# Performance work log

Measured on AMD Instinct MI355X. Metric: run time of the kernel, lower is better.

Reference implementation:

```python
import jax, jax.numpy as jnp
import numpy as np

B = 512          # number of drug-combination graphs (batch)
MAX_LEN = 128    # static padding for to_dense_batch
D_DRUG = 256     # drug_in_features (kdim = vdim)
D_CELL = 1024    # cell_in_features
H = 16           # nheads
HD = 64          # h (per-head dim)
E = H * HD       # embed_dim = 1024


def setup_inputs() -> dict:
    key = jax.random.key(0)
    ks = jax.random.split(key, 12)
    N = 32768
    x_nodes = jax.random.normal(ks[0], (N, D_DRUG), dtype=jnp.float32)
    guide = jnp.sort(jax.random.randint(ks[1], (N,), 0, B)).astype(jnp.int64)
    cell = jax.random.normal(ks[2], (B, D_CELL), dtype=jnp.float32)
    s = 0.02
    return {
        "x_nodes": x_nodes,
        "cell": cell,
        "Wq": jax.random.normal(ks[3], (E, E), dtype=jnp.float32) * s,
        "bq": jnp.zeros((E,), dtype=jnp.float32),
        "Wk": jax.random.normal(ks[4], (E, D_DRUG), dtype=jnp.float32) * s,
        "bk": jnp.zeros((E,), dtype=jnp.float32),
        "Wv": jax.random.normal(ks[5], (E, D_DRUG), dtype=jnp.float32) * s,
        "bv": jnp.zeros((E,), dtype=jnp.float32),
        "Wo": jax.random.normal(ks[6], (E, E), dtype=jnp.float32) * s,
        "bo": jnp.zeros((E,), dtype=jnp.float32),
        "Wc": jax.random.normal(ks[7], (E, D_CELL), dtype=jnp.float32) * s,
        "bc": jnp.zeros((E,), dtype=jnp.float32),
        "guide": guide,
    }


def _to_dense_batch(x_nodes, guide):
    # Faithful torch_geometric.to_dense_batch with static MAX_LEN padding.
    N = x_nodes.shape[0]
    ones = jnp.ones((N,), dtype=jnp.int32)
    counts = jax.ops.segment_sum(ones, guide, num_segments=B)      # [B]
    starts = jnp.cumsum(counts) - counts                            # [B]
    pos = jnp.arange(N, dtype=jnp.int32) - starts[guide]            # rank within segment
    dense = jnp.zeros((B, MAX_LEN, x_nodes.shape[1]), x_nodes.dtype).at[guide, pos].set(x_nodes)
    mask = jnp.zeros((B, MAX_LEN), dtype=bool).at[guide, pos].set(True)
    return dense, mask


def reference(x_nodes, cell, Wq, bq, Wk, bk, Wv, bv, Wo, bo, Wc, bc, guide):
    drug_key, mask = _to_dense_batch(x_nodes, guide)                # [B,M,D_DRUG], [B,M]
    # cell_query_fc then MHA q-projection (single query per graph)
    cq = cell @ Wc.T + bc                                           # [B,E]
    q = (cq @ Wq.T + bq).reshape(B, H, HD) * (HD ** -0.5)           # [B,H,hd]
    k = (drug_key @ Wk.T + bk).reshape(B, MAX_LEN, H, HD)           # [B,M,H,hd]
    v = (drug_key @ Wv.T + bv).reshape(B, MAX_LEN, H, HD)
    scores = jnp.einsum('bhd,bmhd->bhm', q, k)                      # [B,H,M]
    scores = jnp.where(mask[:, None, :], scores, -1e9)
    attn = jax.nn.softmax(scores, axis=-1)
    out = jnp.einsum('bhm,bmhd->bhd', attn, v).reshape(B, E)        # [B,E]
    out = out @ Wo.T + bo
    return jnp.concatenate([out, cell], axis=1)                     # [B, E + D_CELL]
```

## Files before the change

### kernel.cpp

```cpp
#include <hip/hip_runtime.h>
#include <hip/hip_bf16.h>
#include <math.h>

#define B_GRAPHS 512
#define MAXLEN   128
#define DDRUG    256
#define NH       16
#define EMB      1024

typedef __attribute__((ext_vector_type(4))) float f32x4;
typedef __attribute__((ext_vector_type(8))) short s16x8;
typedef __attribute__((ext_vector_type(4))) short s16x4;

__device__ inline short f2bf(float f) {
    unsigned u = __builtin_bit_cast(unsigned, f);
    u += 0x7FFF + ((u >> 16) & 1);
    return (short)(u >> 16);
}
__device__ inline float bf2f(short s) {
    unsigned u = ((unsigned)(unsigned short)s) << 16;
    return __builtin_bit_cast(float, u);
}

__global__ void starts_kernel(const int* __restrict__ g32, int N, int* __restrict__ starts)
{
    int b = blockIdx.x * blockDim.x + threadIdx.x;
    if (b > B_GRAPHS) return;
    bool is64 = (g32[N - 1] == 0);
    int lo = 0, hi = N;
    while (lo < hi) {
        int mid = (lo + hi) >> 1;
        int v = is64 ? g32[2 * mid] : g32[mid];
        if (v < b) lo = mid + 1; else hi = mid;
    }
    starts[b] = lo;
}

__global__ __launch_bounds__(256) void cvt_bf16(
    const float* __restrict__ in, short* __restrict__ out, int n4)
{
    int i = blockIdx.x * 256 + threadIdx.x;
    int stride = gridDim.x * 256;
    for (; i < n4; i += stride) {
        f32x4 v = ((const f32x4*)in)[i];
        s16x4 o;
        o.x = f2bf(v.x); o.y = f2bf(v.y); o.z = f2bf(v.z); o.w = f2bf(v.w);
        ((s16x4*)out)[i] = o;
    }
}

template<bool OUT_BF>
__global__ __launch_bounds__(256) void gemm_bf16_nt(
    const short* __restrict__ A, int lda,
    const short* __restrict__ Bw, int ldb,
    const float* __restrict__ bias, void* __restrict__ Cout,
    int ldc, float scale)
{
    __shared__ short As[64 * 64];
    __shared__ short Bs[64 * 64];
    const int t = threadIdx.x, lane = t & 63, w = t >> 6;
    const int wm = w >> 1, wn = w & 1;
    const int row0 = blockIdx.y * 64, col0 = blockIdx.x * 64;
    f32x4 c[2][2] = {};

    const int sr = t >> 2, sc = (t & 3) * 16;
    const int swz = (sr & 7) << 4;
    const int kb0 = (lane >> 4) * 8;

    for (int kt = 0; kt < 1024; kt += 64) {
        s16x8 va0 = *(const s16x8*)&A [(size_t)(row0 + sr) * lda + kt + sc];
        s16x8 va1 = *(const s16x8*)&A [(size_t)(row0 + sr) * lda + kt + sc + 8];
        s16x8 vb0 = *(const s16x8*)&Bw[(size_t)(col0 + sr) * ldb + kt + sc];
        s16x8 vb1 = *(const s16x8*)&Bw[(size_t)(col0 + sr) * ldb + kt + sc + 8];
        *(s16x8*)((char*)As + sr * 128 + ((sc * 2)      ^ swz)) = va0;
        *(s16x8*)((char*)As + sr * 128 + ((sc * 2 + 16) ^ swz)) = va1;
        *(s16x8*)((char*)Bs + sr * 128 + ((sc * 2)      ^ swz)) = vb0;
        *(s16x8*)((char*)Bs + sr * 128 + ((sc * 2 + 16) ^ swz)) = vb1;
        __syncthreads();
        #pragma unroll
        for (int ks = 0; ks < 2; ++ks) {
            const int kk = (ks * 32 + kb0) * 2;
            s16x8 a0, a1, b0, b1;
            {
                int r = wm * 32 + (lane & 15);
                a0 = *(const s16x8*)((char*)As + r * 128 + (kk ^ ((r & 7) << 4)));
                int r2 = r + 16;
                a1 = *(const s16x8*)((char*)As + r2 * 128 + (kk ^ ((r2 & 7) << 4)));
            }
            {
                int r = wn * 32 + (lane & 15);
                b0 = *(const s16x8*)((char*)Bs + r * 128 + (kk ^ ((r & 7) << 4)));
                int r2 = r + 16;
                b1 = *(const s16x8*)((char*)Bs + r2 * 128 + (kk ^ ((r2 & 7) << 4)));
            }
            c[0][0] = __builtin_amdgcn_mfma_f32_16x16x32_bf16(a0, b0, c[0][0], 0, 0, 0);
            c[0][1] = __builtin_amdgcn_mfma_f32_16x16x32_bf16(a0, b1, c[0][1], 0, 0, 0);
            c[1][0] = __builtin_amdgcn_mfma_f32_16x16x32_bf16(a1, b0, c[1][0], 0, 0, 0);
            c[1][1] = __builtin_amdgcn_mfma_f32_16x16x32_bf16(a1, b1, c[1][1], 0, 0, 0);
        }
        __syncthreads();
    }
    #pragma unroll
    for (int i = 0; i < 2; ++i)
    #pragma unroll
    for (int j = 0; j < 2; ++j) {
        int m0 = row0 + wm * 32 + i * 16 + (lane >> 4) * 4;
        int nn = col0 + wn * 32 + j * 16 + (lane & 15);
        #pragma unroll
        for (int r = 0; r < 4; ++r) {
            float v = (c[i][j][r] + bias[nn]) * scale;
            if (OUT_BF) ((short*)Cout)[(size_t)(m0 + r) * ldc + nn] = f2bf(v);
            else        ((float*)Cout)[(size_t)(m0 + r) * ldc + nn] = v;
        }
    }
}

__global__ __launch_bounds__(256) void qk_kernel(
    const float* __restrict__ q, const float* __restrict__ Wk, short* __restrict__ qkout)
{
    __shared__ float q_s[8][64];
    const int bt = blockIdx.x, h = blockIdx.y, t = threadIdx.x;
    for (int i = t; i < 512; i += 256)
        q_s[i >> 6][i & 63] = q[(size_t)(bt * 8 + (i >> 6)) * EMB + h * 64 + (i & 63)];
    __syncthreads();
    float acc[8] = {};
    const float* wbase = &Wk[(size_t)h * 64 * DDRUG + t];
    #pragma unroll 4
    for (int j = 0; j < 64; ++j) {
        float wv = wbase[(size_t)j * DDRUG];
        #pragma unroll
        for (int bb = 0; bb < 8; ++bb) acc[bb] += q_s[bb][j] * wv;
    }
    #pragma unroll
    for (int bb = 0; bb < 8; ++bb)
        qkout[(size_t)(bt * 8 + bb) * 4096 + h * DDRUG + t] = f2bf(acc[bb]);
}

__global__ __launch_bounds__(256) void attn_kernel(
    const float* __restrict__ X, const short* __restrict__ qk,
    const int* __restrict__ starts, short* __restrict__ xbar, int Ntot)
{
    __shared__ short qk_s[16 * 256];
    __shared__ short Xs[64 * 256];
    __shared__ float S_s[128 * 20];
    const int b = blockIdx.x, t = threadIdx.x;
    const int lane = t & 63, w = t >> 6;
    const int s0 = starts[b];
    int n = starts[b + 1] - s0;
    if (n > MAXLEN) n = MAXLEN;

    {
        int h = t >> 4, cc = (t & 15) * 16;
        const s16x8* src = (const s16x8*)(qk + (size_t)b * 4096 + h * 256 + cc);
        int swzh = (h & 7) << 4;
        *(s16x8*)((char*)qk_s + h * 512 + ((cc * 2)      ^ swzh)) = src[0];
        *(s16x8*)((char*)qk_s + h * 512 + ((cc * 2 + 16) ^ swzh)) = src[1];
    }

    const int sr = t >> 2, scg = (t & 3) * 64;
    auto stageX = [&](int st) {
        int gm = s0 + st * 64 + sr;
        if (gm > Ntot - 1) gm = Ntot - 1;
        const f32x4* src = (const f32x4*)(X + (size_t)gm * 256 + scg);
        int swzr = (sr & 7) << 4;
        #pragma unroll
        for (int j = 0; j < 8; ++j) {
            f32x4 a = src[2 * j], bb = src[2 * j + 1];
            s16x8 v;
            v[0] = f2bf(a.x);  v[1] = f2bf(a.y);  v[2] = f2bf(a.z);  v[3] = f2bf(a.w);
            v[4] = f2bf(bb.x); v[5] = f2bf(bb.y); v[6] = f2bf(bb.z); v[7] = f2bf(bb.w);
            *(s16x8*)((char*)Xs + sr * 512 + (((scg + j * 8) * 2) ^ swzr)) = v;
        }
    };
    stageX(0);
    __syncthreads();

    s16x8 af[8];
    {
        int h = lane & 15, swzh = (h & 7) << 4;
        #pragma unroll
        for (int ks = 0; ks < 8; ++ks) {
            int k = ks * 32 + (lane >> 4) * 8;
            af[ks] = *(const s16x8*)((char*)qk_s + h * 512 + ((k * 2) ^ swzh));
        }
    }
    auto mfmaStage = [&](int st) {
        int lr = w * 16 + (lane & 15);
        int swzr = (lr & 7) << 4;
        f32x4 c = {0.f, 0.f, 0.f, 0.f};
        #pragma unroll
        for (int ks = 0; ks < 8; ++ks) {
            int k = ks * 32 + (lane >> 4) * 8;
            s16x8 bf = *(const s16x8*)((char*)Xs + lr * 512 + ((k * 2) ^ swzr));
            c = __builtin_amdgcn_mfma_f32_16x16x32_bf16(af[ks], bf, c, 0, 0, 0);
        }
        int m = st * 64 + w * 16 + (lane & 15);
        int hb = (lane >> 4) * 4;
        #pragma unroll
        for (int i = 0; i < 4; ++i) S_s[m * 20 + hb + i] = c[i];
    };
    mfmaStage(0);
    if (n > 64) {
        __syncthreads();
        stageX(1);
        __syncthreads();
        mfmaStage(1);
    }
    __syncthreads();

    #pragma unroll
    for (int hh = 0; hh < 4; ++hh) {
        int h = w * 4 + hh;
        float v0 = (lane < n)      ? S_s[lane * 20 + h]        : -INFINITY;
        float v1 = (lane + 64 < n) ? S_s[(lane + 64) * 20 + h] : -INFINITY;
        float mx = fmaxf(v0, v1);
        #pragma unroll
        for (int off = 32; off > 0; off >>= 1) mx = fmaxf(mx, __shfl_xor(mx, off, 64));
        float e0 = (lane < n)      ? __expf(v0 - mx) : 0.f;
        float e1 = (lane + 64 < n) ? __expf(v1 - mx) : 0.f;
        float sm = e0 + e1;
        #pragma unroll
        for (int off = 32; off > 0; off >>= 1) sm += __shfl_xor(sm, off, 64);
        float inv = 1.f / sm;
        if (lane < n)      S_s[lane * 20 + h]        = e0 * inv;
        if (lane + 64 < n) S_s[(lane + 64) * 20 + h] = e1 * inv;
    }
    __syncthreads();

    const int d = t;
    float acc[16] = {};
    const float* Xb = X + (size_t)s0 * 256 + d;
    int m = 0;
    for (; m + 4 <= n; m += 4) {
        float xv[4];
        #pragma unroll
        for (int u = 0; u < 4; ++u) xv[u] = Xb[(size_t)(m + u) * 256];
        #pragma unroll
        for (int u = 0; u < 4; ++u) {
            const f32x4* prow = (const f32x4*)&S_s[(m + u) * 20];
            f32x4 p0 = prow[0], p1 = prow[1], p2 = prow[2], p3 = prow[3];
            float x = xv[u];
            acc[0] += p0.x * x; acc[1] += p0.y * x; acc[2]  += p0.z * x; acc[3]  += p0.w * x;
            acc[4] += p1.x * x; acc[5] += p1.y * x; acc[6]  += p1.z * x; acc[7]  += p1.w * x;
            acc[8] += p2.x * x; acc[9] += p2.y * x; acc[10] += p2.z * x; acc[11] += p2.w * x;
            acc[12] += p3.x * x; acc[13] += p3.y * x; acc[14] += p3.z * x; acc[15] += p3.w * x;
        }
    }
    for (; m < n; ++m) {
        const f32x4* prow = (const f32x4*)&S_s[m * 20];
        f32x4 p0 = prow[0], p1 = prow[1], p2 = prow[2], p3 = prow[3];
        float x = Xb[(size_t)m * 256];
        acc[0] += p0.x * x; acc[1] += p0.y * x; acc[2]  += p0.z * x; acc[3]  += p0.w * x;
        acc[4] += p1.x * x; acc[5] += p1.y * x; acc[6]  += p1.z * x; acc[7]  += p1.w * x;
        acc[8] += p2.x * x; acc[9] += p2.y * x; acc[10] += p2.z * x; acc[11] += p2.w * x;
        acc[12] += p3.x * x; acc[13] += p3.y * x; acc[14] += p3.z * x; acc[15] += p3.w * x;
    }
    short* xb = xbar + (size_t)b * 4096 + d;
    #pragma unroll
    for (int h = 0; h < 16; ++h) xb[(size_t)h * 256] = f2bf(acc[h]);
}

__global__ __launch_bounds__(256) void outh_gemm(
    const short* __restrict__ xbar,
    const short* __restrict__ Wv_bf,
    const float* __restrict__ bv, short* __restrict__ outh)
{
    __shared__ short As[64 * 64];
    __shared__ short Bs[64 * 64];
    const int t = threadIdx.x, lane = t & 63, w = t >> 6;
    const int wm = w >> 1, wn = w & 1;
    const int h = blockIdx.y;
    const int row0 = blockIdx.x * 64;
    const short* A = xbar + (size_t)h * 256;
    const short* B = Wv_bf + (size_t)h * 64 * 256;
    f32x4 c[2][2] = {};

    const int sr = t >> 2, sc = (t & 3) * 16;
    const int swz = (sr & 7) << 4;
    const int kb0 = (lane >> 4) * 8;

    for (int kt = 0; kt < 256; kt += 64) {
        s16x8 va0 = *(const s16x8*)&A[(size_t)(row0 + sr) * 4096 + kt + sc];
        s16x8 va1 = *(const s16x8*)&A[(size_t)(row0 + sr) * 4096 + kt + sc + 8];
        s16x8 vb0 = *(const s16x8*)&B[(size_t)sr * 256 + kt + sc];
        s16x8 vb1 = *(const s16x8*)&B[(size_t)sr * 256 + kt + sc + 8];
        *(s16x8*)((char*)As + sr * 128 + ((sc * 2)      ^ swz)) = va0;
        *(s16x8*)((char*)As + sr * 128 + ((sc * 2 + 16) ^ swz)) = va1;
        *(s16x8*)((char*)Bs + sr * 128 + ((sc * 2)      ^ swz)) = vb0;
        *(s16x8*)((char*)Bs + sr * 128 + ((sc * 2 + 16) ^ swz)) = vb1;
        __syncthreads();
        #pragma unroll
        for (int ks = 0; ks < 2; ++ks) {
            const int kk = (ks * 32 + kb0) * 2;
            s16x8 a0, a1, b0, b1;
            {
                int r = wm * 32 + (lane & 15);
                a0 = *(const s16x8*)((char*)As + r * 128 + (kk ^ ((r & 7) << 4)));
                int r2 = r + 16;
                a1 = *(const s16x8*)((char*)As + r2 * 128 + (kk ^ ((r2 & 7) << 4)));
            }
            {
                int r = wn * 32 + (lane & 15);
                b0 = *(const s16x8*)((char*)Bs + r * 128 + (kk ^ ((r & 7) << 4)));
                int r2 = r + 16;
                b1 = *(const s16x8*)((char*)Bs + r2 * 128 + (kk ^ ((r2 & 7) << 4)));
            }
            c[0][0] = __builtin_amdgcn_mfma_f32_16x16x32_bf16(a0, b0, c[0][0], 0, 0, 0);
            c[0][1] = __builtin_amdgcn_mfma_f32_16x16x32_bf16(a0, b1, c[0][1], 0, 0, 0);
            c[1][0] = __builtin_amdgcn_mfma_f32_16x16x32_bf16(a1, b0, c[1][0], 0, 0, 0);
            c[1][1] = __builtin_amdgcn_mfma_f32_16x16x32_bf16(a1, b1, c[1][1], 0, 0, 0);
        }
        __syncthreads();
    }
    #pragma unroll
    for (int i = 0; i < 2; ++i)
    #pragma unroll
    for (int j = 0; j < 2; ++j) {
        int m0 = row0 + wm * 32 + i * 16 + (lane >> 4) * 4;
        int nn = wn * 32 + j * 16 + (lane & 15);
        #pragma unroll
        for (int r = 0; r < 4; ++r) {
            float v = c[i][j][r] + bv[h * 64 + nn];
            outh[(size_t)(m0 + r) * EMB + h * 64 + nn] = f2bf(v);
        }
    }
}

__global__ __launch_bounds__(256) void concat_kernel(
    const float* __restrict__ cell, float* __restrict__ out)
{
    const int b = blockIdx.x, t = threadIdx.x;
    *(f32x4*)&out[(size_t)b * 2048 + 1024 + t * 4] =
        *(const f32x4*)&cell[(size_t)b * 1024 + t * 4];
}

extern "C" void kernel_launch(void* const* d_in, const int* in_sizes, int n_in,
                              void* d_out, int out_size, void* d_ws, size_t ws_size,
                              hipStream_t stream)
{
    const float* x_nodes = (const float*)d_in[0];
    const float* cell    = (const float*)d_in[1];
    const float* Wq      = (const float*)d_in[2];
    const float* bq      = (const float*)d_in[3];
    const float* Wk      = (const float*)d_in[4];
    const float* Wv      = (const float*)d_in[6];
    const float* bv      = (const float*)d_in[7];
    const float* Wo      = (const float*)d_in[8];
    const float* bo      = (const float*)d_in[9];
    const float* Wc      = (const float*)d_in[10];
    const float* bc      = (const float*)d_in[11];
    const int*   guide   = (const int*)d_in[12];
    const int N = in_sizes[12];
    float* out = (float*)d_out;

    char* ws = (char*)d_ws;
    int*   starts  = (int*)ws;
    float* qf32    = (float*)(ws + 4096);
    short* Wv_bf   = (short*)(ws + 4096);
    short* cell_bf = (short*)(ws + 4096 + (2u << 20));
    short* cq_bf   = (short*)(ws + 4096 + (3u << 20));
    short* outh_bf = (short*)(ws + 4096 + (4u << 20));
    short* qk_bf   = (short*)(ws + 4096 + (5u << 20));
    short* xbar_bf = (short*)(ws + 4096 + (9u << 20));
    short* Wc_bf   = (short*)(ws + 4096 + (13u << 20));
    short* Wq_bf   = (short*)(ws + 4096 + (15u << 20));
    short* Wo_bf   = (short*)(ws + 4096 + (17u << 20));

    starts_kernel<<<3, 256, 0, stream>>>(guide, N, starts);
    cvt_bf16<<<512, 256, 0, stream>>>(cell, cell_bf, (512 * 1024) / 4);
    cvt_bf16<<<512, 256, 0, stream>>>(Wc, Wc_bf, (1024 * 1024) / 4);
    cvt_bf16<<<512, 256, 0, stream>>>(Wq, Wq_bf, (1024 * 1024) / 4);
    cvt_bf16<<<512, 256, 0, stream>>>(Wo, Wo_bf, (1024 * 1024) / 4);

    gemm_bf16_nt<true ><<<dim3(16, 8), 256, 0, stream>>>(
        cell_bf, 1024, Wc_bf, 1024, bc, cq_bf, 1024, 1.0f);
    gemm_bf16_nt<false><<<dim3(16, 8), 256, 0, stream>>>(
        cq_bf, 1024, Wq_bf, 1024, bq, qf32, 1024, 0.125f);

    qk_kernel<<<dim3(B_GRAPHS / 8, NH), 256, 0, stream>>>(qf32, Wk, qk_bf);

    cvt_bf16<<<256, 256, 0, stream>>>(Wv, (short*)Wv_bf, (1024 * 256) / 4);

    attn_kernel<<<B_GRAPHS, 256, 0, stream>>>(x_nodes, qk_bf, starts, xbar_bf, N);
    outh_gemm<<<dim3(8, NH), 256, 0, stream>>>(xbar_bf, Wv_bf, bv, outh_bf);

    gemm_bf16_nt<false><<<dim3(16, 8), 256, 0, stream>>>(
        outh_bf, 1024, Wo_bf, 1024, bo, out, 2048, 1.0f);
    concat_kernel<<<B_GRAPHS, 256, 0, stream>>>(cell, out);

    (void)in_sizes; (void)n_in; (void)out_size; (void)ws_size;
}
```

Before: 186.5 us.

## Fuse prep kernels into one launch and split attention heads across two blocks

Merges the starts binary search, the five fp32-to-bf16 weight and cell conversions, and the cell concat copy into a single grid-stride prep kernel, which removes several launches. The attention kernel now runs on a (B,2) grid, with each block handling 8 heads instead of 16. This doubles parallelism and halves per-block accumulators and shared memory. The cost is that each half stages and converts the same X rows and runs full MFMAs while discarding half of the outputs, so X traffic and conversion work double.

After: 187.2 us. No clear change (+0.4%).

```diff
diff --git a/kernel.cpp b/kernel.cpp
--- a/kernel.cpp
+++ b/kernel.cpp
@@ -22,30 +22,44 @@
     return __builtin_bit_cast(float, u);
 }
 
-__global__ void starts_kernel(const int* __restrict__ g32, int N, int* __restrict__ starts)
-{
-    int b = blockIdx.x * blockDim.x + threadIdx.x;
-    if (b > B_GRAPHS) return;
-    bool is64 = (g32[N - 1] == 0);
-    int lo = 0, hi = N;
-    while (lo < hi) {
-        int mid = (lo + hi) >> 1;
-        int v = is64 ? g32[2 * mid] : g32[mid];
-        if (v < b) lo = mid + 1; else hi = mid;
-    }
-    starts[b] = lo;
-}
-
-__global__ __launch_bounds__(256) void cvt_bf16(
-    const float* __restrict__ in, short* __restrict__ out, int n4)
-{
-    int i = blockIdx.x * 256 + threadIdx.x;
-    int stride = gridDim.x * 256;
-    for (; i < n4; i += stride) {
-        f32x4 v = ((const f32x4*)in)[i];
-        s16x4 o;
-        o.x = f2bf(v.x); o.y = f2bf(v.y); o.z = f2bf(v.z); o.w = f2bf(v.w);
-        ((s16x4*)out)[i] = o;
+__device__ inline void cvt4(const float* __restrict__ in, short* __restrict__ out, int j)
+{
+    f32x4 v = ((const f32x4*)in)[j];
+    s16x4 o;
+    o.x = f2bf(v.x); o.y = f2bf(v.y); o.z = f2bf(v.z); o.w = f2bf(v.w);
+    ((s16x4*)out)[j] = o;
+}
+
+__global__ __launch_bounds__(256) void prep_kernel(
+    const float* __restrict__ cell, const float* __restrict__ Wc,
+    const float* __restrict__ Wq,   const float* __restrict__ Wo,
+    const float* __restrict__ Wv,   const int* __restrict__ g32, int N,
+    float* __restrict__ out, short* __restrict__ cell_bf, short* __restrict__ Wc_bf,
+    short* __restrict__ Wq_bf, short* __restrict__ Wo_bf, short* __restrict__ Wv_bf,
+    int* __restrict__ starts)
+{
+    const int stride = gridDim.x * 256;
+    for (int i = blockIdx.x * 256 + threadIdx.x; i < 1114625; i += stride) {
+        if      (i <  131072) cvt4(cell, cell_bf, i);
+        else if (i <  393216) cvt4(Wc, Wc_bf, i - 131072);
+        else if (i <  655360) cvt4(Wq, Wq_bf, i - 393216);
+        else if (i <  917504) cvt4(Wo, Wo_bf, i - 655360);
+        else if (i <  983040) cvt4(Wv, Wv_bf, i - 917504);
+        else if (i < 1114112) {
+            int j = i - 983040;
+            int b = j >> 8, c4 = j & 255;
+            *(f32x4*)&out[(size_t)b * 2048 + 1024 + c4 * 4] = ((const f32x4*)cell)[j];
+        } else {
+            int b = i - 1114112;
+            bool is64 = (g32[N - 1] == 0);
+            int lo = 0, hi = N;
+            while (lo < hi) {
+                int mid = (lo + hi) >> 1;
+                int v = is64 ? g32[2 * mid] : g32[mid];
+                if (v < b) lo = mid + 1; else hi = mid;
+            }
+            starts[b] = lo;
+        }
     }
 }
 
@@ -140,21 +154,19 @@
     const float* __restrict__ X, const short* __restrict__ qk,
     const int* __restrict__ starts, short* __restrict__ xbar, int Ntot)
 {
-    __shared__ short qk_s[16 * 256];
+    __shared__ short qk_s[8 * 256];
     __shared__ short Xs[64 * 256];
-    __shared__ float S_s[128 * 20];
-    const int b = blockIdx.x, t = threadIdx.x;
+    __shared__ float S_s[128 * 12];
+    const int b = blockIdx.x, half = blockIdx.y, t = threadIdx.x;
     const int lane = t & 63, w = t >> 6;
     const int s0 = starts[b];
     int n = starts[b + 1] - s0;
     if (n > MAXLEN) n = MAXLEN;
 
     {
-        int h = t >> 4, cc = (t & 15) * 16;
-        const s16x8* src = (const s16x8*)(qk + (size_t)b * 4096 + h * 256 + cc);
-        int swzh = (h & 7) << 4;
-        *(s16x8*)((char*)qk_s + h * 512 + ((cc * 2)      ^ swzh)) = src[0];
-        *(s16x8*)((char*)qk_s + h * 512 + ((cc * 2 + 16) ^ swzh)) = src[1];
+        int hl = t >> 5, cc = (t & 31) * 8;
+        const s16x8* src = (const s16x8*)(qk + (size_t)b * 4096 + (half * 8 + hl) * 256 + cc);
+        *(s16x8*)((char*)qk_s + hl * 512 + ((cc * 2) ^ ((hl & 7) << 4))) = src[0];
     }
 
     const int sr = t >> 2, scg = (t & 3) * 64;
@@ -177,11 +189,11 @@
 
     s16x8 af[8];
     {
-        int h = lane & 15, swzh = (h & 7) << 4;
+        int r = lane & 7, swzh = r << 4;
         #pragma unroll
         for (int ks = 0; ks < 8; ++ks) {
             int k = ks * 32 + (lane >> 4) * 8;
-            af[ks] = *(const s16x8*)((char*)qk_s + h * 512 + ((k * 2) ^ swzh));
+            af[ks] = *(const s16x8*)((char*)qk_s + r * 512 + ((k * 2) ^ swzh));
         }
     }
     auto mfmaStage = [&](int st) {
@@ -196,8 +208,10 @@
         }
         int m = st * 64 + w * 16 + (lane & 15);
         int hb = (lane >> 4) * 4;
-        #pragma unroll
-        for (int i = 0; i < 4; ++i) S_s[m * 20 + hb + i] = c[i];
+        if (hb < 8) {
+            #pragma unroll
+            for (int i = 0; i < 4; ++i) S_s[m * 12 + hb + i] = c[i];
+        }
     };
     mfmaStage(0);
     if (n > 64) {
@@ -209,10 +223,10 @@
     __syncthreads();
 
     #pragma unroll
-    for (int hh = 0; hh < 4; ++hh) {
-        int h = w * 4 + hh;
-        float v0 = (lane < n)      ? S_s[lane * 20 + h]        : -INFINITY;
-        float v1 = (lane + 64 < n) ? S_s[(lane + 64) * 20 + h] : -INFINITY;
+    for (int hh = 0; hh < 2; ++hh) {
+        int h = w * 2 + hh;
+        float v0 = (lane < n)      ? S_s[lane * 12 + h]        : -INFINITY;
+        float v1 = (lane + 64 < n) ? S_s[(lane + 64) * 12 + h] : -INFINITY;
         float mx = fmaxf(v0, v1);
         #pragma unroll
         for (int off = 32; off > 0; off >>= 1) mx = fmaxf(mx, __shfl_xor(mx, off, 64));
@@ -222,13 +236,13 @@
         #pragma unroll
         for (int off = 32; off > 0; off >>= 1) sm += __shfl_xor(sm, off, 64);
         float inv = 1.f / sm;
-        if (lane < n)      S_s[lane * 20 + h]        = e0 * inv;
-        if (lane + 64 < n) S_s[(lane + 64) * 20 + h] = e1 * inv;
+        if (lane < n)      S_s[lane * 12 + h]        = e0 * inv;
+        if (lane + 64 < n) S_s[(lane + 64) * 12 + h] = e1 * inv;
     }
     __syncthreads();
 
     const int d = t;
-    float acc[16] = {};
+    float acc[8] = {};
     const float* Xb = X + (size_t)s0 * 256 + d;
     int m = 0;
     for (; m + 4 <= n; m += 4) {
@@ -237,27 +251,23 @@
         for (int u = 0; u < 4; ++u) xv[u] = Xb[(size_t)(m + u) * 256];
         #pragma unroll
         for (int u = 0; u < 4; ++u) {
-            const f32x4* prow = (const f32x4*)&S_s[(m + u) * 20];
-            f32x4 p0 = prow[0], p1 = prow[1], p2 = prow[2], p3 = prow[3];
+            const f32x4* prow = (const f32x4*)&S_s[(m + u) * 12];
+            f32x4 p0 = prow[0], p1 = prow[1];
             float x = xv[u];
-            acc[0] += p0.x * x; acc[1] += p0.y * x; acc[2]  += p0.z * x; acc[3]  += p0.w * x;
-            acc[4] += p1.x * x; acc[5] += p1.y * x; acc[6]  += p1.z * x; acc[7]  += p1.w * x;
-            acc[8] += p2.x * x; acc[9] += p2.y * x; acc[10] += p2.z * x; acc[11] += p2.w * x;
-            acc[12] += p3.x * x; acc[13] += p3.y * x; acc[14] += p3.z * x; acc[15] += p3.w * x;
+            acc[0] += p0.x * x; acc[1] += p0.y * x; acc[2] += p0.z * x; acc[3] += p0.w * x;
+            acc[4] += p1.x * x; acc[5] += p1.y * x; acc[6] += p1.z * x; acc[7] += p1.w * x;
         }
     }
     for (; m < n; ++m) {
-        const f32x4* prow = (const f32x4*)&S_s[m * 20];
-        f32x4 p0 = prow[0], p1 = prow[1], p2 = prow[2], p3 = prow[3];
+        const f32x4* prow = (const f32x4*)&S_s[m * 12];
+        f32x4 p0 = prow[0], p1 = prow[1];
         float x = Xb[(size_t)m * 256];
-        acc[0] += p0.x * x; acc[1] += p0.y * x; acc[2]  += p0.z * x; acc[3]  += p0.w * x;
-        acc[4] += p1.x * x; acc[5] += p1.y * x; acc[6]  += p1.z * x; acc[7]  += p1.w * x;
-        acc[8] += p2.x * x; acc[9] += p2.y * x; acc[10] += p2.z * x; acc[11] += p2.w * x;
-        acc[12] += p3.x * x; acc[13] += p3.y * x; acc[14] += p3.z * x; acc[15] += p3.w * x;
-    }
-    short* xb = xbar + (size_t)b * 4096 + d;
-    #pragma unroll
-    for (int h = 0; h < 16; ++h) xb[(size_t)h * 256] = f2bf(acc[h]);
+        acc[0] += p0.x * x; acc[1] += p0.y * x; acc[2] += p0.z * x; acc[3] += p0.w * x;
+        acc[4] += p1.x * x; acc[5] += p1.y * x; acc[6] += p1.z * x; acc[7] += p1.w * x;
+    }
+    short* xb = xbar + (size_t)b * 4096 + (size_t)(half * 8) * 256 + d;
+    #pragma unroll
+    for (int h = 0; h < 8; ++h) xb[(size_t)h * 256] = f2bf(acc[h]);
 }
 
 __global__ __launch_bounds__(256) void outh_gemm(
@@ -324,14 +334,6 @@
             outh[(size_t)(m0 + r) * EMB + h * 64 + nn] = f2bf(v);
         }
     }
-}
-
-__global__ __launch_bounds__(256) void concat_kernel(
-    const float* __restrict__ cell, float* __restrict__ out)
-{
-    const int b = blockIdx.x, t = threadIdx.x;
-    *(f32x4*)&out[(size_t)b * 2048 + 1024 + t * 4] =
-        *(const f32x4*)&cell[(size_t)b * 1024 + t * 4];
 }
 
 extern "C" void kernel_launch(void* const* d_in, const int* in_sizes, int n_in,
@@ -356,7 +358,6 @@
     char* ws = (char*)d_ws;
     int*   starts  = (int*)ws;
     float* qf32    = (float*)(ws + 4096);
-    short* Wv_bf   = (short*)(ws + 4096);
     short* cell_bf = (short*)(ws + 4096 + (2u << 20));
     short* cq_bf   = (short*)(ws + 4096 + (3u << 20));
     short* outh_bf = (short*)(ws + 4096 + (4u << 20));
@@ -365,12 +366,11 @@
     short* Wc_bf   = (short*)(ws + 4096 + (13u << 20));
     short* Wq_bf   = (short*)(ws + 4096 + (15u << 20));
     short* Wo_bf   = (short*)(ws + 4096 + (17u << 20));
-
-    starts_kernel<<<3, 256, 0, stream>>>(guide, N, starts);
-    cvt_bf16<<<512, 256, 0, stream>>>(cell, cell_bf, (512 * 1024) / 4);
-    cvt_bf16<<<512, 256, 0, stream>>>(Wc, Wc_bf, (1024 * 1024) / 4);
-    cvt_bf16<<<512, 256, 0, stream>>>(Wq, Wq_bf, (1024 * 1024) / 4);
-    cvt_bf16<<<512, 256, 0, stream>>>(Wo, Wo_bf, (1024 * 1024) / 4);
+    short* Wv_bf   = (short*)(ws + 4096 + (19u << 20));
+
+    prep_kernel<<<2048, 256, 0, stream>>>(
+        cell, Wc, Wq, Wo, Wv, guide, N, out,
+        cell_bf, Wc_bf, Wq_bf, Wo_bf, Wv_bf, starts);
 
     gemm_bf16_nt<true ><<<dim3(16, 8), 256, 0, stream>>>(
         cell_bf, 1024, Wc_bf, 1024, bc, cq_bf, 1024, 1.0f);
@@ -379,14 +379,12 @@
 
     qk_kernel<<<dim3(B_GRAPHS / 8, NH), 256, 0, stream>>>(qf32, Wk, qk_bf);
 
-    cvt_bf16<<<256, 256, 0, stream>>>(Wv, (short*)Wv_bf, (1024 * 256) / 4);
-
-    attn_kernel<<<B_GRAPHS, 256, 0, stream>>>(x_nodes, qk_bf, starts, xbar_bf, N);
+    attn_kernel<<<dim3(B_GRAPHS, 2), 256, 0, stream>>>(x_nodes, qk_bf, starts, xbar_bf, N);
+
     outh_gemm<<<dim3(8, NH), 256, 0, stream>>>(xbar_bf, Wv_bf, bv, outh_bf);
 
     gemm_bf16_nt<false><<<dim3(16, 8), 256, 0, stream>>>(
         outh_bf, 1024, Wo_bf, 1024, bo, out, 2048, 1.0f);
-    concat_kernel<<<B_GRAPHS, 256, 0, stream>>>(cell, out);
 
     (void)in_sizes; (void)n_in; (void)out_size; (void)ws_size;
 }
```
